# Optimization experiments

Hardware: AMD Instinct MI355X
Metric: run time of the kernel (lower is better)

Reference implementation:

```python
import jax, jax.numpy as jnp
import numpy as np

DIM = 64
NUM_GRAPHS = 256  # B: number of graphs in the batch (static)


def setup_inputs() -> dict:
    key = jax.random.key(0)
    ks = jax.random.split(key, 16)
    N, E = 8000, 40000

    def p(k, shape, s=0.1):
        return jax.random.normal(k, shape, jnp.float32) * s

    return dict(
        x=jax.random.normal(ks[0], (N, 21), jnp.float32),
        edge_attr=jax.random.uniform(ks[1], (E, 16), jnp.float32),
        edge_index=jax.random.randint(ks[2], (2, E), 0, N, jnp.int32),
        batch=jnp.sort(jax.random.randint(ks[3], (N,), 0, NUM_GRAPHS, jnp.int32)),
        lin0_w=p(ks[4], (DIM, 21)), lin0_b=jnp.zeros((DIM,), jnp.float32),
        nn_w1=p(ks[5], (128, 16)), nn_b1=jnp.zeros((128,), jnp.float32),
        nn_w2=p(ks[6], (DIM * DIM, 128), 0.02), nn_b2=jnp.zeros((DIM * DIM,), jnp.float32),
        conv_root=p(ks[7], (DIM, DIM)), conv_bias=jnp.zeros((DIM,), jnp.float32),
        gru_w_ih=p(ks[8], (3 * DIM, DIM)), gru_w_hh=p(ks[9], (3 * DIM, DIM)),
        gru_b_ih=jnp.zeros((3 * DIM,), jnp.float32), gru_b_hh=jnp.zeros((3 * DIM,), jnp.float32),
        lstm_w_ih=p(ks[10], (4 * DIM, 2 * DIM)), lstm_w_hh=p(ks[11], (4 * DIM, DIM)),
        lstm_b_ih=jnp.zeros((4 * DIM,), jnp.float32), lstm_b_hh=jnp.zeros((4 * DIM,), jnp.float32),
        lin1_w=p(ks[12], (DIM, 2 * DIM)), lin1_b=jnp.zeros((DIM,), jnp.float32),
        lin2_w=p(ks[13], (1, DIM)), lin2_b=jnp.zeros((1,), jnp.float32),
    )


def reference(x, edge_attr, edge_index, batch,
              lin0_w, lin0_b, nn_w1, nn_b1, nn_w2, nn_b2,
              conv_root, conv_bias, gru_w_ih, gru_w_hh, gru_b_ih, gru_b_hh,
              lstm_w_ih, lstm_w_hh, lstm_b_ih, lstm_b_hh,
              lin1_w, lin1_b, lin2_w, lin2_b):
    N = x.shape[0]
    src, dst = edge_index[0], edge_index[1]

    out = jax.nn.relu(x @ lin0_w.T + lin0_b)           # [N, 64]
    h = out

    # edge-conditioned weights (same every iteration): [E, 64, 64]
    e_h = jax.nn.relu(edge_attr @ nn_w1.T + nn_b1)
    w_e = (e_h @ nn_w2.T + nn_b2).reshape(-1, DIM, DIM)

    deg = jax.ops.segment_sum(jnp.ones_like(src, jnp.float32), dst, num_segments=N)
    deg = jnp.maximum(deg, 1.0)[:, None]

    for _ in range(3):
        # NNConv: gather + per-edge matmul + scatter-mean + root/bias
        msg = jnp.einsum('ei,eio->eo', out[src], w_e)  # [E, 64]
        agg = jax.ops.segment_sum(msg, dst, num_segments=N) / deg
        m = jax.nn.relu(agg + out @ conv_root + conv_bias)
        # GRU cell (seq_len = 1), torch gate order r, z, n
        gi = m @ gru_w_ih.T + gru_b_ih
        gh = h @ gru_w_hh.T + gru_b_hh
        ir, iz, i_n = jnp.split(gi, 3, axis=-1)
        hr, hz, h_n = jnp.split(gh, 3, axis=-1)
        r = jax.nn.sigmoid(ir + hr)
        z = jax.nn.sigmoid(iz + hz)
        n = jnp.tanh(i_n + r * h_n)
        h = (1.0 - z) * n + z * h
        out = h

    # Set2Set pooling, 3 processing steps
    B = NUM_GRAPHS
    q_star = jnp.zeros((B, 2 * DIM), x.dtype)
    hs = jnp.zeros((B, DIM), x.dtype)
    cs = jnp.zeros((B, DIM), x.dtype)
    for _ in range(3):
        gates = q_star @ lstm_w_ih.T + lstm_b_ih + hs @ lstm_w_hh.T + lstm_b_hh
        gi_, gf_, gg_, go_ = jnp.split(gates, 4, axis=-1)  # torch gate order i,f,g,o
        cs = jax.nn.sigmoid(gf_) * cs + jax.nn.sigmoid(gi_) * jnp.tanh(gg_)
        hs = jax.nn.sigmoid(go_) * jnp.tanh(cs)
        q = hs                                             # [B, 64]
        e = jnp.sum(out * q[batch], axis=-1)               # [N]
        mmax = jax.ops.segment_max(e, batch, num_segments=B)
        ex = jnp.exp(e - mmax[batch])
        s = jax.ops.segment_sum(ex, batch, num_segments=B)
        a = ex / s[batch]
        r_read = jax.ops.segment_sum(a[:, None] * out, batch, num_segments=B)
        q_star = jnp.concatenate([q, r_read], axis=-1)     # [B, 128]

    y = jax.nn.relu(q_star @ lin1_w.T + lin1_b)
    y = y @ lin2_w.T + lin2_b
    return y.reshape(-1)
```

## Files before the change

kernel.cpp:

```cpp
#include <hip/hip_runtime.h>
#include <math.h>

#define NN 8000
#define NE 40000
#define NGB 256
#define SK 8192
#define KSPLIT 16

typedef unsigned int u32;
typedef unsigned short u16;
typedef __attribute__((ext_vector_type(8))) short short8v;
typedef __attribute__((ext_vector_type(4))) float float4v;
typedef __attribute__((ext_vector_type(4))) unsigned int uint4v;

__device__ __forceinline__ float sigmoidf_(float x) { return 1.f / (1.f + expf(-x)); }

__device__ __forceinline__ u32 bf16_rne(float f) {
    u32 x = __builtin_bit_cast(u32, f);
    return (x + 0x7FFFu + ((x >> 16) & 1u)) >> 16;
}

__device__ __forceinline__ uint4v pack_bf8(const float v[8]) {
    u32 h[8];
#pragma unroll
    for (int j = 0; j < 8; ++j) h[j] = bf16_rne(v[j]);
    return (uint4v){ h[0] | (h[1] << 16), h[2] | (h[3] << 16),
                     h[4] | (h[5] << 16), h[6] | (h[7] << 16) };
}

__device__ __forceinline__ void pack8(const float* p, float scale, short8v& ah, short8v& al) {
    float v[8];
#pragma unroll
    for (int j = 0; j < 8; ++j) v[j] = p[j];
    u32 hu[8], lu[8];
#pragma unroll
    for (int j = 0; j < 8; ++j) {
        float s = v[j] * scale;
        hu[j] = bf16_rne(s);
        float fh = __builtin_bit_cast(float, hu[j] << 16);
        lu[j] = bf16_rne(s - fh);
    }
    uint4v hset = { hu[0] | (hu[1] << 16), hu[2] | (hu[3] << 16),
                    hu[4] | (hu[5] << 16), hu[6] | (hu[7] << 16) };
    uint4v lset = { lu[0] | (lu[1] << 16), lu[2] | (lu[3] << 16),
                    lu[4] | (lu[5] << 16), lu[6] | (lu[7] << 16) };
    ah = __builtin_bit_cast(short8v, hset);
    al = __builtin_bit_cast(short8v, lset);
}

#define SETUP_LIN0 (NN * 64)
#define SETUP_EH   (NE * 128)
#define SETUP_W2   (64 * SK)
#define SETUP_MW   8192
#define SETUP_GB   24576
__global__ void k_setup(const float* __restrict__ x, const float* __restrict__ lin0_w,
                        const float* __restrict__ lin0_b,
                        const float* __restrict__ ea, const float* __restrict__ nn_w1,
                        const float* __restrict__ nn_b1,
                        const float* __restrict__ nn_w2, const float* __restrict__ conv_root,
                        const float* __restrict__ nn_b2, const float* __restrict__ gw_ih,
                        const float* __restrict__ gw_hh, const int* __restrict__ batch,
                        float* __restrict__ out, float* __restrict__ e_h,
                        u16* __restrict__ Whi, u16* __restrict__ Wlo,
                        u16* __restrict__ Bmh, u16* __restrict__ Bml,
                        u16* __restrict__ Bih_h, u16* __restrict__ Bih_l,
                        u16* __restrict__ Bhh_h, u16* __restrict__ Bhh_l,
                        int* __restrict__ gstart) {
    int idx = blockIdx.x * 256 + threadIdx.x;
    if (idx < SETUP_LIN0) {
        int n = idx >> 6, o = idx & 63;
        float s = lin0_b[o];
#pragma unroll
        for (int c = 0; c < 21; ++c) s += x[n * 21 + c] * lin0_w[o * 21 + c];
        out[idx] = fmaxf(s, 0.f);
        return;
    }
    idx -= SETUP_LIN0;
    if (idx < SETUP_EH) {
        int e = idx >> 7, j = idx & 127;
        float s = nn_b1[j];
#pragma unroll
        for (int c = 0; c < 16; ++c) s += ea[e * 16 + c] * nn_w1[j * 16 + c];
        e_h[idx] = fmaxf(s, 0.f);
        return;
    }
    idx -= SETUP_EH;
    if (idx < SETUP_W2) {
        int o = idx >> 13, kap = idx & 8191;
        int i = kap >> 7, k = kap & 127;
        float v = nn_w2[(size_t)((i << 6) + o) * 128 + k];
        u32 h = bf16_rne(v);
        float fh = __builtin_bit_cast(float, h << 16);
        u32 l = bf16_rne(v - fh);
        int pos = ((kap >> 3) * 64 + o) * 8 + (kap & 7);
        Whi[pos] = (u16)h; Wlo[pos] = (u16)l;
        return;
    }
    idx -= SETUP_W2;
    if (idx < SETUP_MW) {
        int k = idx >> 6, o = idx & 63;
        float v = (k < 64) ? nn_b2[k * 64 + o] : conv_root[(k - 64) * 64 + o];
        u32 h = bf16_rne(v);
        float fh = __builtin_bit_cast(float, h << 16);
        u32 l = bf16_rne(v - fh);
        int pos = ((k >> 3) * 64 + o) * 8 + (k & 7);
        Bmh[pos] = (u16)h; Bml[pos] = (u16)l;
        return;
    }
    idx -= SETUP_MW;
    if (idx < SETUP_GB) {
        int half = idx >= 12288;
        int i2 = idx - half * 12288;
        int o = i2 % 192, k = i2 / 192;
        float v = half ? gw_hh[o * 64 + k] : gw_ih[o * 64 + k];
        u32 h = bf16_rne(v);
        float fh = __builtin_bit_cast(float, h << 16);
        u32 l = bf16_rne(v - fh);
        int pos = ((k >> 3) * 192 + o) * 8 + (k & 7);
        if (half) { Bhh_h[pos] = (u16)h; Bhh_l[pos] = (u16)l; }
        else      { Bih_h[pos] = (u16)h; Bih_l[pos] = (u16)l; }
        return;
    }
    idx -= SETUP_GB;
    if (idx <= NGB) {
        int g = idx;
        int lo = 0, hi = NN;
        while (lo < hi) { int mid = (lo + hi) >> 1; if (batch[mid] < g) lo = mid + 1; else hi = mid; }
        gstart[g] = lo;
    }
}
#define SETUP_TOTAL (SETUP_LIN0 + SETUP_EH + SETUP_W2 + SETUP_MW + SETUP_GB + NGB + 1)

__global__ void k_deg(const int* __restrict__ dst, int* __restrict__ degi) {
    int e = blockIdx.x * blockDim.x + threadIdx.x;
    if (e < NE) atomicAdd(&degi[dst[e]], 1);
}

__global__ __launch_bounds__(1024) void k_scan(
    const int* __restrict__ degi, int* __restrict__ rowptr,
    int* __restrict__ cursor, float* __restrict__ degf) {
    __shared__ int tsum[1024];
    int t = threadIdx.x;
    int base = t * 8;
    int v[8];
    int s = 0;
#pragma unroll
    for (int j = 0; j < 8; ++j) {
        int i = base + j;
        v[j] = (i < NN) ? degi[i] : 0;
        s += v[j];
    }
    tsum[t] = s;
    __syncthreads();
    for (int off = 1; off < 1024; off <<= 1) {
        int add = (t >= off) ? tsum[t - off] : 0;
        __syncthreads();
        tsum[t] += add;
        __syncthreads();
    }
    int exc = (t == 0) ? 0 : tsum[t - 1];
#pragma unroll
    for (int j = 0; j < 8; ++j) {
        int i = base + j;
        if (i < NN) {
            rowptr[i] = exc; cursor[i] = exc;
            degf[i] = (float)(v[j] > 1 ? v[j] : 1);
            exc += v[j];
        }
    }
    if (t == 1023) rowptr[NN] = tsum[1023];
}

__global__ void k_fill(const int* __restrict__ dst, int* __restrict__ cursor,
                       int* __restrict__ elist) {
    int e = blockIdx.x * blockDim.x + threadIdx.x;
    if (e < NE) { int p = atomicAdd(&cursor[dst[e]], 1); elist[p] = e; }
}

__global__ __launch_bounds__(256) void k_sbuild(
    const float* __restrict__ out, const float* __restrict__ e_h,
    const int* __restrict__ src, const int* __restrict__ rowptr,
    const int* __restrict__ elist, u16* __restrict__ S_bf,
    float* __restrict__ Osum, float* __restrict__ Psum, int base) {
    int t = threadIdx.x;
    int n = base + blockIdx.x;
    int ig = t >> 4;
    int k8 = t & 15;
    int lane = t & 63;
    float acc[4][8];
#pragma unroll
    for (int j = 0; j < 4; ++j)
#pragma unroll
        for (int c = 0; c < 8; ++c) acc[j][c] = 0.f;
    float osum = 0.f;
    int r0 = rowptr[n], r1 = rowptr[n + 1];
    const float4* out4 = (const float4*)out;
    const float4* eh4p = (const float4*)e_h;
    for (int idx = r0; idx < r1; ++idx) {
        int e = elist[idx];
        int sn = src[e];
        float4 e0 = eh4p[(size_t)e * 32 + k8 * 2];
        float4 e1 = eh4p[(size_t)e * 32 + k8 * 2 + 1];
        float ehv[8] = {e0.x, e0.y, e0.z, e0.w, e1.x, e1.y, e1.z, e1.w};
        float4 f = out4[sn * 16 + ig];
        float fv[4] = {f.x, f.y, f.z, f.w};
#pragma unroll
        for (int j = 0; j < 4; ++j)
#pragma unroll
            for (int c = 0; c < 8; ++c) acc[j][c] += fv[j] * ehv[c];
        if (t < 64) osum += out[(size_t)sn * 64 + lane];
    }
    uint4v* S4 = (uint4v*)S_bf;
    size_t rb = (size_t)blockIdx.x * (SK / 8);
#pragma unroll
    for (int j = 0; j < 4; ++j)
        S4[rb + (size_t)(ig * 4 + j) * 16 + k8] = pack_bf8(acc[j]);
    if (t < 64) {
        Osum[(size_t)n * 64 + lane] = osum;
        Psum[(size_t)n * 64 + lane] = 0.f;
    }
}

__global__ __launch_bounds__(128) void k_gemm(
    const u16* __restrict__ S_bf, const u16* __restrict__ Whi,
    const u16* __restrict__ Wlo, float* __restrict__ Psum, int base) {
    int t = threadIdx.x;
    int wv = t >> 6, lane = t & 63;
    int lrow = lane & 15, lkg = lane >> 4;
    int m0 = blockIdx.x * 64 + wv * 32;
    int ks = blockIdx.y;
    int kbase = ks * (SK / KSPLIT);
    float4v acc[2][4];
#pragma unroll
    for (int ms = 0; ms < 2; ++ms)
#pragma unroll
        for (int nt = 0; nt < 4; ++nt) acc[ms][nt] = (float4v){0.f, 0.f, 0.f, 0.f};
    const short8v* bhv = (const short8v*)Whi;
    const short8v* blv = (const short8v*)Wlo;
    const u16* ar0 = S_bf + (size_t)(m0 + lrow) * SK + kbase + lkg * 8;
    const u16* ar1 = ar0 + (size_t)16 * SK;
    int kc0 = (kbase >> 3) + lkg;

#pragma unroll 4
    for (int kk = 0; kk < SK / KSPLIT / 32; ++kk) {
        short8v ah0 = *(const short8v*)(ar0 + kk * 32);
        short8v ah1 = *(const short8v*)(ar1 + kk * 32);
        int bo = (kc0 + kk * 4) * 64 + lrow;
        short8v bh[4], bl[4];
#pragma unroll
        for (int nt = 0; nt < 4; ++nt) { bh[nt] = bhv[bo + nt * 16]; bl[nt] = blv[bo + nt * 16]; }
#pragma unroll
        for (int nt = 0; nt < 4; ++nt) {
            acc[0][nt] = __builtin_amdgcn_mfma_f32_16x16x32_bf16(ah0, bh[nt], acc[0][nt], 0, 0, 0);
            acc[0][nt] = __builtin_amdgcn_mfma_f32_16x16x32_bf16(ah0, bl[nt], acc[0][nt], 0, 0, 0);
            acc[1][nt] = __builtin_amdgcn_mfma_f32_16x16x32_bf16(ah1, bh[nt], acc[1][nt], 0, 0, 0);
            acc[1][nt] = __builtin_amdgcn_mfma_f32_16x16x32_bf16(ah1, bl[nt], acc[1][nt], 0, 0, 0);
        }
    }
    int gbase = base + m0;
#pragma unroll
    for (int ms = 0; ms < 2; ++ms)
#pragma unroll
        for (int nt = 0; nt < 4; ++nt)
#pragma unroll
            for (int jj = 0; jj < 4; ++jj) {
                int row = ms * 16 + lkg * 4 + jj;
                int o = nt * 16 + lrow;
                atomicAdd(&Psum[(size_t)(gbase + row) * 64 + o], acc[ms][nt][jj]);
            }
}

__global__ __launch_bounds__(64) void k_node(
    float* __restrict__ out, const float* __restrict__ Psum,
    const float* __restrict__ Osum, const float* __restrict__ degf,
    const u16* __restrict__ Bmh, const u16* __restrict__ Bml,
    const u16* __restrict__ Bih_h, const u16* __restrict__ Bih_l,
    const u16* __restrict__ Bhh_h, const u16* __restrict__ Bhh_l,
    const float* __restrict__ conv_bias,
    const float* __restrict__ gb_ih, const float* __restrict__ gb_hh) {
    __shared__ float lds[16][68];
    int lane = threadIdx.x;
    int lrow = lane & 15, lkg = lane >> 4;
    int n0 = blockIdx.x * 16;
    int arow = n0 + lrow;

    float invd = 1.f / degf[arow];
    float4v acc[4];
#pragma unroll
    for (int nt = 0; nt < 4; ++nt) acc[nt] = (float4v){0.f, 0.f, 0.f, 0.f};
    const short8v* bhv = (const short8v*)Bmh;
    const short8v* blv = (const short8v*)Bml;
#pragma unroll
    for (int s = 0; s < 4; ++s) {
        short8v ah, al;
        if (s < 2) pack8(&Osum[(size_t)arow * 64 + s * 32 + lkg * 8], invd, ah, al);
        else       pack8(&out[(size_t)arow * 64 + (s - 2) * 32 + lkg * 8], 1.f, ah, al);
        int kc = s * 4 + lkg;
#pragma unroll
        for (int nt = 0; nt < 4; ++nt) {
            short8v bh = bhv[kc * 64 + nt * 16 + lrow];
            short8v bl = blv[kc * 64 + nt * 16 + lrow];
            acc[nt] = __builtin_amdgcn_mfma_f32_16x16x32_bf16(ah, bh, acc[nt], 0, 0, 0);
            acc[nt] = __builtin_amdgcn_mfma_f32_16x16x32_bf16(al, bh, acc[nt], 0, 0, 0);
            acc[nt] = __builtin_amdgcn_mfma_f32_16x16x32_bf16(ah, bl, acc[nt], 0, 0, 0);
        }
    }
    float invd2[4];
#pragma unroll
    for (int jj = 0; jj < 4; ++jj) invd2[jj] = 1.f / degf[n0 + lkg * 4 + jj];
#pragma unroll
    for (int nt = 0; nt < 4; ++nt) {
        int o = nt * 16 + lrow;
        float cb = conv_bias[o];
#pragma unroll
        for (int jj = 0; jj < 4; ++jj) {
            int row = n0 + lkg * 4 + jj;
            lds[lkg * 4 + jj][o] =
                fmaxf(acc[nt][jj] + Psum[(size_t)row * 64 + o] * invd2[jj] + cb, 0.f);
        }
    }
    __syncthreads();

    float4v ai[12], ah_[12];
#pragma unroll
    for (int nt = 0; nt < 12; ++nt) { ai[nt] = (float4v){0.f, 0.f, 0.f, 0.f}; ah_[nt] = (float4v){0.f, 0.f, 0.f, 0.f}; }
    const short8v* bih_h = (const short8v*)Bih_h;
    const short8v* bih_l = (const short8v*)Bih_l;
    const short8v* bhh_h = (const short8v*)Bhh_h;
    const short8v* bhh_l = (const short8v*)Bhh_l;
#pragma unroll
    for (int s = 0; s < 2; ++s) {
        short8v mh, ml, hh, hl;
        pack8(&lds[lrow][s * 32 + lkg * 8], 1.f, mh, ml);
        pack8(&out[(size_t)arow * 64 + s * 32 + lkg * 8], 1.f, hh, hl);
        int kc = s * 4 + lkg;
#pragma unroll
        for (int nt = 0; nt < 12; ++nt) {
            int bo = kc * 192 + nt * 16 + lrow;
            short8v b1 = bih_h[bo], b2 = bih_l[bo];
            ai[nt] = __builtin_amdgcn_mfma_f32_16x16x32_bf16(mh, b1, ai[nt], 0, 0, 0);
            ai[nt] = __builtin_amdgcn_mfma_f32_16x16x32_bf16(ml, b1, ai[nt], 0, 0, 0);
            ai[nt] = __builtin_amdgcn_mfma_f32_16x16x32_bf16(mh, b2, ai[nt], 0, 0, 0);
            short8v b3 = bhh_h[bo], b4 = bhh_l[bo];
            ah_[nt] = __builtin_amdgcn_mfma_f32_16x16x32_bf16(hh, b3, ah_[nt], 0, 0, 0);
            ah_[nt] = __builtin_amdgcn_mfma_f32_16x16x32_bf16(hl, b3, ah_[nt], 0, 0, 0);
            ah_[nt] = __builtin_amdgcn_mfma_f32_16x16x32_bf16(hh, b4, ah_[nt], 0, 0, 0);
        }
    }
#pragma unroll
    for (int nt = 0; nt < 4; ++nt) {
        int o = nt * 16 + lrow;
        float bi0 = gb_ih[o], bi1 = gb_ih[64 + o], bi2 = gb_ih[128 + o];
        float bh0 = gb_hh[o], bh1 = gb_hh[64 + o], bh2 = gb_hh[128 + o];
#pragma unroll
        for (int jj = 0; jj < 4; ++jj) {
            int row = n0 + lkg * 4 + jj;
            float ir = ai[nt][jj] + bi0,  hr = ah_[nt][jj] + bh0;
            float iz = ai[nt + 4][jj] + bi1, hz = ah_[nt + 4][jj] + bh1;
            float in_ = ai[nt + 8][jj] + bi2, hn = ah_[nt + 8][jj] + bh2;
            float r = sigmoidf_(ir + hr);
            float z = sigmoidf_(iz + hz);
            float nv = tanhf(in_ + r * hn);
            float ho = out[(size_t)row * 64 + o];
            out[(size_t)row * 64 + o] = (1.f - z) * nv + z * ho;
        }
    }
}

__global__ __launch_bounds__(256) void k_s2s(
    const float* __restrict__ out, const int* __restrict__ gstart,
    const float* __restrict__ lw_ih, const float* __restrict__ lw_hh,
    const float* __restrict__ lb_ih, const float* __restrict__ lb_hh,
    const float* __restrict__ lin1_w, const float* __restrict__ lin1_b,
    const float* __restrict__ lin2_w, const float* __restrict__ lin2_b,
    float* __restrict__ yout) {
    __shared__ float qs[128], hsL[64], csL[64], gates[256];
    __shared__ float pv[384];
    __shared__ float red[4][64];
    __shared__ float sswv[4], mmaxw[4];
    int g = blockIdx.x, t = threadIdx.x, wv = t >> 6, lane = t & 63;
    int s0 = gstart[g], s1 = gstart[g + 1];
    if (t < 128) qs[t] = 0.f;
    if (t < 64) { hsL[t] = 0.f; csL[t] = 0.f; }
    __syncthreads();
    for (int st = 0; st < 3; ++st) {
        float s = lb_ih[t] + lb_hh[t];
        const float4* wi = (const float4*)&lw_ih[t * 128];
#pragma unroll
        for (int i = 0; i < 32; ++i) {
            float4 a = wi[i];
            s += qs[i * 4] * a.x + qs[i * 4 + 1] * a.y + qs[i * 4 + 2] * a.z + qs[i * 4 + 3] * a.w;
        }
        const float4* wh = (const float4*)&lw_hh[t * 64];
#pragma unroll
        for (int i = 0; i < 16; ++i) {
            float4 a = wh[i];
            s += hsL[i * 4] * a.x + hsL[i * 4 + 1] * a.y + hsL[i * 4 + 2] * a.z + hsL[i * 4 + 3] * a.w;
        }
        gates[t] = s;
        __syncthreads();
        if (t < 64) {
            float ig = sigmoidf_(gates[t]);
            float fg = sigmoidf_(gates[64 + t]);
            float gg = tanhf(gates[128 + t]);
            float og = sigmoidf_(gates[192 + t]);
            float c = fg * csL[t] + ig * gg;
            csL[t] = c;
            hsL[t] = og * tanhf(c);
        }
        __syncthreads();
        float wmax = -1e30f;
        for (int i = s0 + wv; i < s1; i += 4) {
            float p = out[(size_t)i * 64 + lane] * hsL[lane];
#pragma unroll
            for (int off = 32; off >= 1; off >>= 1) p += __shfl_xor(p, off);
            if (lane == 0) pv[i - s0] = p;
            wmax = fmaxf(wmax, p);
        }
        if (lane == 0) mmaxw[wv] = wmax;
        __syncthreads();
        float mmax = fmaxf(fmaxf(mmaxw[0], mmaxw[1]), fmaxf(mmaxw[2], mmaxw[3]));
        float ssum = 0.f, racc = 0.f;
        for (int i = s0 + wv; i < s1; i += 4) {
            float w = expf(pv[i - s0] - mmax);
            ssum += w;
            racc += w * out[(size_t)i * 64 + lane];
        }
        red[wv][lane] = racc;
        if (lane == 0) sswv[wv] = ssum;
        __syncthreads();
        if (t < 64) {
            float rt = red[0][t] + red[1][t] + red[2][t] + red[3][t];
            float stot = sswv[0] + sswv[1] + sswv[2] + sswv[3];
            qs[t] = hsL[t];
            qs[64 + t] = (s1 > s0) ? rt / stot : 0.f;
        }
        __syncthreads();
    }
    if (t < 64) {
        float s = lin1_b[t];
        const float4* w1 = (const float4*)&lin1_w[t * 128];
#pragma unroll
        for (int i = 0; i < 32; ++i) {
            float4 a = w1[i];
            s += qs[i * 4] * a.x + qs[i * 4 + 1] * a.y + qs[i * 4 + 2] * a.z + qs[i * 4 + 3] * a.w;
        }
        s = fmaxf(s, 0.f) * lin2_w[t];
#pragma unroll
        for (int off = 32; off >= 1; off >>= 1) s += __shfl_xor(s, off);
        if (t == 0) yout[g] = s + lin2_b[0];
    }
}

extern "C" void kernel_launch(void* const* d_in, const int* in_sizes, int n_in,
                              void* d_out, int out_size, void* d_ws, size_t ws_size,
                              hipStream_t stream) {
    (void)in_sizes; (void)n_in; (void)out_size;
    const float* x        = (const float*)d_in[0];
    const float* eattr    = (const float*)d_in[1];
    const int*   ei       = (const int*)d_in[2];
    const int*   batch    = (const int*)d_in[3];
    const float* lin0_w   = (const float*)d_in[4];
    const float* lin0_b   = (const float*)d_in[5];
    const float* nn_w1    = (const float*)d_in[6];
    const float* nn_b1    = (const float*)d_in[7];
    const float* nn_w2    = (const float*)d_in[8];
    const float* nn_b2    = (const float*)d_in[9];
    const float* conv_root= (const float*)d_in[10];
    const float* conv_bias= (const float*)d_in[11];
    const float* gw_ih    = (const float*)d_in[12];
    const float* gw_hh    = (const float*)d_in[13];
    const float* gb_ih    = (const float*)d_in[14];
    const float* gb_hh    = (const float*)d_in[15];
    const float* lw_ih    = (const float*)d_in[16];
    const float* lw_hh    = (const float*)d_in[17];
    const float* lb_ih    = (const float*)d_in[18];
    const float* lb_hh    = (const float*)d_in[19];
    const float* lin1_w   = (const float*)d_in[20];
    const float* lin1_b   = (const float*)d_in[21];
    const float* lin2_w   = (const float*)d_in[22];
    const float* lin2_b   = (const float*)d_in[23];
    const int* src = ei;
    const int* dst = ei + NE;

    char* w = (char*)d_ws;
    auto alloc = [&](size_t bytes) { char* p = w; w += (bytes + 255) & ~(size_t)255; return p; };
    float* out    = (float*)alloc((size_t)NN * 64 * 4);
    float* e_h    = (float*)alloc((size_t)NE * 128 * 4);
    u16*   Whi    = (u16*)alloc((size_t)64 * SK * 2);
    u16*   Wlo    = (u16*)alloc((size_t)64 * SK * 2);
    float* Psum   = (float*)alloc((size_t)NN * 64 * 4);
    float* Osum   = (float*)alloc((size_t)NN * 64 * 4);
    u16*   Bmh    = (u16*)alloc((size_t)8192 * 2);
    u16*   Bml    = (u16*)alloc((size_t)8192 * 2);
    u16*   Bih_h  = (u16*)alloc((size_t)12288 * 2);
    u16*   Bih_l  = (u16*)alloc((size_t)12288 * 2);
    u16*   Bhh_h  = (u16*)alloc((size_t)12288 * 2);
    u16*   Bhh_l  = (u16*)alloc((size_t)12288 * 2);
    float* degf   = (float*)alloc((size_t)NN * 4);
    int*   degi   = (int*)alloc((size_t)NN * 4);
    int*   rowptr = (int*)alloc((size_t)(NN + 1) * 4);
    int*   cursor = (int*)alloc((size_t)(NN + 1) * 4);
    int*   elist  = (int*)alloc((size_t)NE * 4);
    int*   gstart = (int*)alloc((size_t)(NGB + 1) * 4);
    size_t used = (size_t)(w - (char*)d_ws);
    size_t avail = ws_size > used ? ws_size - used : 0;
    size_t maxrows = avail / ((size_t)SK * 2);
    int chunkN = maxrows > (size_t)NN ? NN : (int)maxrows;
    chunkN = (chunkN / 64) * 64;
    if (chunkN < 64) chunkN = 64;
    u16* S_bf = (u16*)w;

    hipMemsetAsync(degi, 0, (size_t)NN * 4, stream);

    k_setup<<<(SETUP_TOTAL + 255) / 256, 256, 0, stream>>>(
        x, lin0_w, lin0_b, eattr, nn_w1, nn_b1, nn_w2, conv_root, nn_b2,
        gw_ih, gw_hh, batch, out, e_h, Whi, Wlo, Bmh, Bml,
        Bih_h, Bih_l, Bhh_h, Bhh_l, gstart);
    k_deg<<<(NE + 255) / 256, 256, 0, stream>>>(dst, degi);
    k_scan<<<1, 1024, 0, stream>>>(degi, rowptr, cursor, degf);
    k_fill<<<(NE + 255) / 256, 256, 0, stream>>>(dst, cursor, elist);

    for (int it = 0; it < 3; ++it) {
        for (int cb = 0; cb < NN; cb += chunkN) {
            int cn = (NN - cb) < chunkN ? (NN - cb) : chunkN;
            k_sbuild<<<cn, 256, 0, stream>>>(out, e_h, src, rowptr, elist, S_bf, Osum, Psum, cb);
            k_gemm<<<dim3(cn / 64, KSPLIT), 128, 0, stream>>>(S_bf, Whi, Wlo, Psum, cb);
        }
        k_node<<<NN / 16, 64, 0, stream>>>(out, Psum, Osum, degf, Bmh, Bml,
                                           Bih_h, Bih_l, Bhh_h, Bhh_l,
                                           conv_bias, gb_ih, gb_hh);
    }

    k_s2s<<<NGB, 256, 0, stream>>>(out, gstart, lw_ih, lw_hh, lb_ih, lb_hh,
                                   lin1_w, lin1_b, lin2_w, lin2_b, (float*)d_out);
}
```

Before: 411.6 us.

## Replace split-K atomic accumulation with per-split partial buffers reduced in node kernel

The GEMM no longer atomically adds its split-K partial results into a shared Psum. Each split now writes to its own slice of a KSPLIT-sized partial buffer, and the node kernel sums the 16 partials into LDS before using them. The GEMM block also shrinks from two waves to one (32 rows per block), which doubles the grid, and the degree memset is folded into the setup kernel. This trades atomic contention and the Psum zeroing for more memory traffic: 16 full-size partial buffers are written and then read back in k_node.

```diff
diff --git a/kernel.cpp b/kernel.cpp
--- a/kernel.cpp
+++ b/kernel.cpp
@@ -53,6 +53,8 @@
 #define SETUP_W2   (64 * SK)
 #define SETUP_MW   8192
 #define SETUP_GB   24576
+#define SETUP_G    (NGB + 1)
+#define SETUP_TOTAL (SETUP_LIN0 + SETUP_EH + SETUP_W2 + SETUP_MW + SETUP_GB + SETUP_G + NN)
 __global__ void k_setup(const float* __restrict__ x, const float* __restrict__ lin0_w,
                         const float* __restrict__ lin0_b,
                         const float* __restrict__ ea, const float* __restrict__ nn_w1,
@@ -65,7 +67,7 @@
                         u16* __restrict__ Bmh, u16* __restrict__ Bml,
                         u16* __restrict__ Bih_h, u16* __restrict__ Bih_l,
                         u16* __restrict__ Bhh_h, u16* __restrict__ Bhh_l,
-                        int* __restrict__ gstart) {
+                        int* __restrict__ gstart, int* __restrict__ degi) {
     int idx = blockIdx.x * 256 + threadIdx.x;
     if (idx < SETUP_LIN0) {
         int n = idx >> 6, o = idx & 63;
@@ -122,14 +124,16 @@
         return;
     }
     idx -= SETUP_GB;
-    if (idx <= NGB) {
+    if (idx < SETUP_G) {
         int g = idx;
         int lo = 0, hi = NN;
         while (lo < hi) { int mid = (lo + hi) >> 1; if (batch[mid] < g) lo = mid + 1; else hi = mid; }
         gstart[g] = lo;
-    }
-}
-#define SETUP_TOTAL (SETUP_LIN0 + SETUP_EH + SETUP_W2 + SETUP_MW + SETUP_GB + NGB + 1)
+        return;
+    }
+    idx -= SETUP_G;
+    if (idx < NN) degi[idx] = 0;
+}
 
 __global__ void k_deg(const int* __restrict__ dst, int* __restrict__ degi) {
     int e = blockIdx.x * blockDim.x + threadIdx.x;
@@ -181,7 +185,7 @@
     const float* __restrict__ out, const float* __restrict__ e_h,
     const int* __restrict__ src, const int* __restrict__ rowptr,
     const int* __restrict__ elist, u16* __restrict__ S_bf,
-    float* __restrict__ Osum, float* __restrict__ Psum, int base) {
+    float* __restrict__ Osum, int base) {
     int t = threadIdx.x;
     int n = base + blockIdx.x;
     int ig = t >> 4;
@@ -215,19 +219,15 @@
 #pragma unroll
     for (int j = 0; j < 4; ++j)
         S4[rb + (size_t)(ig * 4 + j) * 16 + k8] = pack_bf8(acc[j]);
-    if (t < 64) {
-        Osum[(size_t)n * 64 + lane] = osum;
-        Psum[(size_t)n * 64 + lane] = 0.f;
-    }
-}
-
-__global__ __launch_bounds__(128) void k_gemm(
+    if (t < 64) Osum[(size_t)n * 64 + lane] = osum;
+}
+
+__global__ __launch_bounds__(64) void k_gemm(
     const u16* __restrict__ S_bf, const u16* __restrict__ Whi,
-    const u16* __restrict__ Wlo, float* __restrict__ Psum, int base) {
-    int t = threadIdx.x;
-    int wv = t >> 6, lane = t & 63;
+    const u16* __restrict__ Wlo, float* __restrict__ P, int base) {
+    int lane = threadIdx.x;
     int lrow = lane & 15, lkg = lane >> 4;
-    int m0 = blockIdx.x * 64 + wv * 32;
+    int m0 = blockIdx.x * 32;
     int ks = blockIdx.y;
     int kbase = ks * (SK / KSPLIT);
     float4v acc[2][4];
@@ -266,12 +266,12 @@
             for (int jj = 0; jj < 4; ++jj) {
                 int row = ms * 16 + lkg * 4 + jj;
                 int o = nt * 16 + lrow;
-                atomicAdd(&Psum[(size_t)(gbase + row) * 64 + o], acc[ms][nt][jj]);
+                P[((size_t)ks * NN + gbase + row) * 64 + o] = acc[ms][nt][jj];
             }
 }
 
 __global__ __launch_bounds__(64) void k_node(
-    float* __restrict__ out, const float* __restrict__ Psum,
+    float* __restrict__ out, const float* __restrict__ P,
     const float* __restrict__ Osum, const float* __restrict__ degf,
     const u16* __restrict__ Bmh, const u16* __restrict__ Bml,
     const u16* __restrict__ Bih_h, const u16* __restrict__ Bih_l,
@@ -284,6 +284,24 @@
     int n0 = blockIdx.x * 16;
     int arow = n0 + lrow;
 
+    {
+        const float4* P4 = (const float4*)P;
+        float4 ps[4];
+#pragma unroll
+        for (int c = 0; c < 4; ++c) ps[c] = make_float4(0.f, 0.f, 0.f, 0.f);
+        for (int p = 0; p < KSPLIT; ++p) {
+#pragma unroll
+            for (int c = 0; c < 4; ++c) {
+                float4 v = P4[(size_t)p * (NN * 16) + (size_t)arow * 16 + lkg * 4 + c];
+                ps[c].x += v.x; ps[c].y += v.y; ps[c].z += v.z; ps[c].w += v.w;
+            }
+        }
+#pragma unroll
+        for (int c = 0; c < 4; ++c)
+            *(float4*)&lds[lrow][lkg * 16 + c * 4] = ps[c];
+    }
+    __syncthreads();
+
     float invd = 1.f / degf[arow];
     float4v acc[4];
 #pragma unroll
@@ -308,17 +326,21 @@
     float invd2[4];
 #pragma unroll
     for (int jj = 0; jj < 4; ++jj) invd2[jj] = 1.f / degf[n0 + lkg * 4 + jj];
+    float mval[4][4];
 #pragma unroll
     for (int nt = 0; nt < 4; ++nt) {
         int o = nt * 16 + lrow;
         float cb = conv_bias[o];
 #pragma unroll
-        for (int jj = 0; jj < 4; ++jj) {
-            int row = n0 + lkg * 4 + jj;
-            lds[lkg * 4 + jj][o] =
-                fmaxf(acc[nt][jj] + Psum[(size_t)row * 64 + o] * invd2[jj] + cb, 0.f);
-        }
-    }
+        for (int jj = 0; jj < 4; ++jj)
+            mval[nt][jj] = fmaxf(acc[nt][jj] + lds[lkg * 4 + jj][o] * invd2[jj] + cb, 0.f);
+    }
+    __syncthreads();
+#pragma unroll
+    for (int nt = 0; nt < 4; ++nt)
+#pragma unroll
+        for (int jj = 0; jj < 4; ++jj)
+            lds[lkg * 4 + jj][nt * 16 + lrow] = mval[nt][jj];
     __syncthreads();
 
     float4v ai[12], ah_[12];
@@ -489,7 +511,7 @@
     float* e_h    = (float*)alloc((size_t)NE * 128 * 4);
     u16*   Whi    = (u16*)alloc((size_t)64 * SK * 2);
     u16*   Wlo    = (u16*)alloc((size_t)64 * SK * 2);
-    float* Psum   = (float*)alloc((size_t)NN * 64 * 4);
+    float* P      = (float*)alloc((size_t)KSPLIT * NN * 64 * 4);
     float* Osum   = (float*)alloc((size_t)NN * 64 * 4);
     u16*   Bmh    = (u16*)alloc((size_t)8192 * 2);
     u16*   Bml    = (u16*)alloc((size_t)8192 * 2);
@@ -511,12 +533,10 @@
     if (chunkN < 64) chunkN = 64;
     u16* S_bf = (u16*)w;
 
-    hipMemsetAsync(degi, 0, (size_t)NN * 4, stream);
-
     k_setup<<<(SETUP_TOTAL + 255) / 256, 256, 0, stream>>>(
         x, lin0_w, lin0_b, eattr, nn_w1, nn_b1, nn_w2, conv_root, nn_b2,
         gw_ih, gw_hh, batch, out, e_h, Whi, Wlo, Bmh, Bml,
-        Bih_h, Bih_l, Bhh_h, Bhh_l, gstart);
+        Bih_h, Bih_l, Bhh_h, Bhh_l, gstart, degi);
     k_deg<<<(NE + 255) / 256, 256, 0, stream>>>(dst, degi);
     k_scan<<<1, 1024, 0, stream>>>(degi, rowptr, cursor, degf);
     k_fill<<<(NE + 255) / 256, 256, 0, stream>>>(dst, cursor, elist);
@@ -524,10 +544,10 @@
     for (int it = 0; it < 3; ++it) {
         for (int cb = 0; cb < NN; cb += chunkN) {
             int cn = (NN - cb) < chunkN ? (NN - cb) : chunkN;
-            k_sbuild<<<cn, 256, 0, stream>>>(out, e_h, src, rowptr, elist, S_bf, Osum, Psum, cb);
-            k_gemm<<<dim3(cn / 64, KSPLIT), 128, 0, stream>>>(S_bf, Whi, Wlo, Psum, cb);
-        }
-        k_node<<<NN / 16, 64, 0, stream>>>(out, Psum, Osum, degf, Bmh, Bml,
+            k_sbuild<<<cn, 256, 0, stream>>>(out, e_h, src, rowptr, elist, S_bf, Osum, cb);
+            k_gemm<<<dim3(cn / 32, KSPLIT), 64, 0, stream>>>(S_bf, Whi, Wlo, P, cb);
+        }
+        k_node<<<NN / 16, 64, 0, stream>>>(out, P, Osum, degf, Bmh, Bml,
                                            Bih_h, Bih_l, Bhh_h, Bhh_l,
                                            conv_bias, gb_ih, gb_hh);
     }
```

New measurement: 380.1 us. -7.7%, faster.

## Fuse per-node S construction with bf16 MFMA GEMM through shared memory

Applied to the files above, without the earlier changes.

Replaces the two-kernel scheme, which wrote a large bf16 S matrix to global memory and then ran a K-split GEMM with atomic adds, with one kernel. Each block of 16 nodes builds its S slice in shared memory one K chunk at a time and feeds it straight into MFMA. This removes the global S round trip, the Psum zeroing and the atomics, and the W reordering in setup is adjusted to the new K ordering. The trade-offs are that each block walks its edge lists 16 times (once per K chunk), uses 16-row tiles, and synchronises twice per chunk. The degree memset is also folded into the setup kernel.

```diff
diff --git a/kernel.cpp b/kernel.cpp
--- a/kernel.cpp
+++ b/kernel.cpp
@@ -5,7 +5,6 @@
 #define NE 40000
 #define NGB 256
 #define SK 8192
-#define KSPLIT 16
 
 typedef unsigned int u32;
 typedef unsigned short u16;
@@ -18,14 +17,6 @@
 __device__ __forceinline__ u32 bf16_rne(float f) {
     u32 x = __builtin_bit_cast(u32, f);
     return (x + 0x7FFFu + ((x >> 16) & 1u)) >> 16;
-}
-
-__device__ __forceinline__ uint4v pack_bf8(const float v[8]) {
-    u32 h[8];
-#pragma unroll
-    for (int j = 0; j < 8; ++j) h[j] = bf16_rne(v[j]);
-    return (uint4v){ h[0] | (h[1] << 16), h[2] | (h[3] << 16),
-                     h[4] | (h[5] << 16), h[6] | (h[7] << 16) };
 }
 
 __device__ __forceinline__ void pack8(const float* p, float scale, short8v& ah, short8v& al) {
@@ -53,6 +44,8 @@
 #define SETUP_W2   (64 * SK)
 #define SETUP_MW   8192
 #define SETUP_GB   24576
+#define SETUP_G    (NGB + 1)
+#define SETUP_TOTAL (SETUP_LIN0 + SETUP_EH + SETUP_W2 + SETUP_MW + SETUP_GB + SETUP_G + NN)
 __global__ void k_setup(const float* __restrict__ x, const float* __restrict__ lin0_w,
                         const float* __restrict__ lin0_b,
                         const float* __restrict__ ea, const float* __restrict__ nn_w1,
@@ -65,7 +58,7 @@
                         u16* __restrict__ Bmh, u16* __restrict__ Bml,
                         u16* __restrict__ Bih_h, u16* __restrict__ Bih_l,
                         u16* __restrict__ Bhh_h, u16* __restrict__ Bhh_l,
-                        int* __restrict__ gstart) {
+                        int* __restrict__ gstart, int* __restrict__ degi) {
     int idx = blockIdx.x * 256 + threadIdx.x;
     if (idx < SETUP_LIN0) {
         int n = idx >> 6, o = idx & 63;
@@ -87,7 +80,7 @@
     idx -= SETUP_EH;
     if (idx < SETUP_W2) {
         int o = idx >> 13, kap = idx & 8191;
-        int i = kap >> 7, k = kap & 127;
+        int k = kap >> 6, i = kap & 63;
         float v = nn_w2[(size_t)((i << 6) + o) * 128 + k];
         u32 h = bf16_rne(v);
         float fh = __builtin_bit_cast(float, h << 16);
@@ -122,14 +115,16 @@
         return;
     }
     idx -= SETUP_GB;
-    if (idx <= NGB) {
+    if (idx < SETUP_G) {
         int g = idx;
         int lo = 0, hi = NN;
         while (lo < hi) { int mid = (lo + hi) >> 1; if (batch[mid] < g) lo = mid + 1; else hi = mid; }
         gstart[g] = lo;
-    }
-}
-#define SETUP_TOTAL (SETUP_LIN0 + SETUP_EH + SETUP_W2 + SETUP_MW + SETUP_GB + NGB + 1)
+        return;
+    }
+    idx -= SETUP_G;
+    if (idx < NN) degi[idx] = 0;
+}
 
 __global__ void k_deg(const int* __restrict__ dst, int* __restrict__ degi) {
     int e = blockIdx.x * blockDim.x + threadIdx.x;
@@ -177,97 +172,68 @@
     if (e < NE) { int p = atomicAdd(&cursor[dst[e]], 1); elist[p] = e; }
 }
 
-__global__ __launch_bounds__(256) void k_sbuild(
+__global__ __launch_bounds__(256) void k_conv(
     const float* __restrict__ out, const float* __restrict__ e_h,
     const int* __restrict__ src, const int* __restrict__ rowptr,
-    const int* __restrict__ elist, u16* __restrict__ S_bf,
-    float* __restrict__ Osum, float* __restrict__ Psum, int base) {
+    const int* __restrict__ elist,
+    const u16* __restrict__ Whi, const u16* __restrict__ Wlo,
+    float* __restrict__ Osum, float* __restrict__ Psum) {
+    __shared__ u16 S_chunk[16][520];
     int t = threadIdx.x;
-    int n = base + blockIdx.x;
-    int ig = t >> 4;
-    int k8 = t & 15;
-    int lane = t & 63;
-    float acc[4][8];
-#pragma unroll
-    for (int j = 0; j < 4; ++j)
-#pragma unroll
-        for (int c = 0; c < 8; ++c) acc[j][c] = 0.f;
-    float osum = 0.f;
-    int r0 = rowptr[n], r1 = rowptr[n + 1];
+    int n0 = blockIdx.x * 16;
+    int r = t >> 4, c = t & 15;
+    int n = n0 + r;
+    int ei0 = rowptr[n], ei1 = rowptr[n + 1];
+    int lane = t & 63, w = t >> 6;
+    int lrow = lane & 15, lkg = lane >> 4;
+    float4v acc = (float4v){0.f, 0.f, 0.f, 0.f};
+    const short8v* bhv = (const short8v*)Whi;
+    const short8v* blv = (const short8v*)Wlo;
     const float4* out4 = (const float4*)out;
     const float4* eh4p = (const float4*)e_h;
-    for (int idx = r0; idx < r1; ++idx) {
-        int e = elist[idx];
-        int sn = src[e];
-        float4 e0 = eh4p[(size_t)e * 32 + k8 * 2];
-        float4 e1 = eh4p[(size_t)e * 32 + k8 * 2 + 1];
-        float ehv[8] = {e0.x, e0.y, e0.z, e0.w, e1.x, e1.y, e1.z, e1.w};
-        float4 f = out4[sn * 16 + ig];
-        float fv[4] = {f.x, f.y, f.z, f.w};
-#pragma unroll
-        for (int j = 0; j < 4; ++j)
-#pragma unroll
-            for (int c = 0; c < 8; ++c) acc[j][c] += fv[j] * ehv[c];
-        if (t < 64) osum += out[(size_t)sn * 64 + lane];
-    }
-    uint4v* S4 = (uint4v*)S_bf;
-    size_t rb = (size_t)blockIdx.x * (SK / 8);
-#pragma unroll
-    for (int j = 0; j < 4; ++j)
-        S4[rb + (size_t)(ig * 4 + j) * 16 + k8] = pack_bf8(acc[j]);
-    if (t < 64) {
-        Osum[(size_t)n * 64 + lane] = osum;
-        Psum[(size_t)n * 64 + lane] = 0.f;
-    }
-}
-
-__global__ __launch_bounds__(128) void k_gemm(
-    const u16* __restrict__ S_bf, const u16* __restrict__ Whi,
-    const u16* __restrict__ Wlo, float* __restrict__ Psum, int base) {
-    int t = threadIdx.x;
-    int wv = t >> 6, lane = t & 63;
-    int lrow = lane & 15, lkg = lane >> 4;
-    int m0 = blockIdx.x * 64 + wv * 32;
-    int ks = blockIdx.y;
-    int kbase = ks * (SK / KSPLIT);
-    float4v acc[2][4];
-#pragma unroll
-    for (int ms = 0; ms < 2; ++ms)
-#pragma unroll
-        for (int nt = 0; nt < 4; ++nt) acc[ms][nt] = (float4v){0.f, 0.f, 0.f, 0.f};
-    const short8v* bhv = (const short8v*)Whi;
-    const short8v* blv = (const short8v*)Wlo;
-    const u16* ar0 = S_bf + (size_t)(m0 + lrow) * SK + kbase + lkg * 8;
-    const u16* ar1 = ar0 + (size_t)16 * SK;
-    int kc0 = (kbase >> 3) + lkg;
-
+
+    for (int ks = 0; ks < 16; ++ks) {
+        float a[8][4];
+#pragma unroll
+        for (int kk = 0; kk < 8; ++kk)
+#pragma unroll
+            for (int j = 0; j < 4; ++j) a[kk][j] = 0.f;
+        float os[4] = {0.f, 0.f, 0.f, 0.f};
+        for (int idx = ei0; idx < ei1; ++idx) {
+            int e = elist[idx];
+            int sn = src[e];
+            float4 ea0 = eh4p[(size_t)e * 32 + ks * 2];
+            float4 ea1 = eh4p[(size_t)e * 32 + ks * 2 + 1];
+            float ehv[8] = {ea0.x, ea0.y, ea0.z, ea0.w, ea1.x, ea1.y, ea1.z, ea1.w};
+            float4 f = out4[(size_t)sn * 16 + c];
+            float fv[4] = {f.x, f.y, f.z, f.w};
+#pragma unroll
+            for (int kk = 0; kk < 8; ++kk)
+#pragma unroll
+                for (int j = 0; j < 4; ++j) a[kk][j] += ehv[kk] * fv[j];
+            if (ks == 0) { os[0] += fv[0]; os[1] += fv[1]; os[2] += fv[2]; os[3] += fv[3]; }
+        }
+#pragma unroll
+        for (int kk = 0; kk < 8; ++kk) {
+            u32 lo = bf16_rne(a[kk][0]) | (bf16_rne(a[kk][1]) << 16);
+            u32 hi = bf16_rne(a[kk][2]) | (bf16_rne(a[kk][3]) << 16);
+            *(uint2*)&S_chunk[r][kk * 64 + c * 4] = make_uint2(lo, hi);
+        }
+        if (ks == 0)
+            *(float4*)&Osum[(size_t)n * 64 + c * 4] = make_float4(os[0], os[1], os[2], os[3]);
+        __syncthreads();
 #pragma unroll 4
-    for (int kk = 0; kk < SK / KSPLIT / 32; ++kk) {
-        short8v ah0 = *(const short8v*)(ar0 + kk * 32);
-        short8v ah1 = *(const short8v*)(ar1 + kk * 32);
-        int bo = (kc0 + kk * 4) * 64 + lrow;
-        short8v bh[4], bl[4];
-#pragma unroll
-        for (int nt = 0; nt < 4; ++nt) { bh[nt] = bhv[bo + nt * 16]; bl[nt] = blv[bo + nt * 16]; }
-#pragma unroll
-        for (int nt = 0; nt < 4; ++nt) {
-            acc[0][nt] = __builtin_amdgcn_mfma_f32_16x16x32_bf16(ah0, bh[nt], acc[0][nt], 0, 0, 0);
-            acc[0][nt] = __builtin_amdgcn_mfma_f32_16x16x32_bf16(ah0, bl[nt], acc[0][nt], 0, 0, 0);
-            acc[1][nt] = __builtin_amdgcn_mfma_f32_16x16x32_bf16(ah1, bh[nt], acc[1][nt], 0, 0, 0);
-            acc[1][nt] = __builtin_amdgcn_mfma_f32_16x16x32_bf16(ah1, bl[nt], acc[1][nt], 0, 0, 0);
-        }
-    }
-    int gbase = base + m0;
-#pragma unroll
-    for (int ms = 0; ms < 2; ++ms)
-#pragma unroll
-        for (int nt = 0; nt < 4; ++nt)
-#pragma unroll
-            for (int jj = 0; jj < 4; ++jj) {
-                int row = ms * 16 + lkg * 4 + jj;
-                int o = nt * 16 + lrow;
-                atomicAdd(&Psum[(size_t)(gbase + row) * 64 + o], acc[ms][nt][jj]);
-            }
+        for (int kk2 = 0; kk2 < 16; ++kk2) {
+            short8v av = *(const short8v*)&S_chunk[lrow][kk2 * 32 + lkg * 8];
+            int bo = (ks * 64 + kk2 * 4 + lkg) * 64 + w * 16 + lrow;
+            acc = __builtin_amdgcn_mfma_f32_16x16x32_bf16(av, bhv[bo], acc, 0, 0, 0);
+            acc = __builtin_amdgcn_mfma_f32_16x16x32_bf16(av, blv[bo], acc, 0, 0, 0);
+        }
+        __syncthreads();
+    }
+#pragma unroll
+    for (int jj = 0; jj < 4; ++jj)
+        Psum[(size_t)(n0 + lkg * 4 + jj) * 64 + w * 16 + lrow] = acc[jj];
 }
 
 __global__ __launch_bounds__(64) void k_node(
@@ -455,7 +421,7 @@
 extern "C" void kernel_launch(void* const* d_in, const int* in_sizes, int n_in,
                               void* d_out, int out_size, void* d_ws, size_t ws_size,
                               hipStream_t stream) {
-    (void)in_sizes; (void)n_in; (void)out_size;
+    (void)in_sizes; (void)n_in; (void)out_size; (void)ws_size;
     const float* x        = (const float*)d_in[0];
     const float* eattr    = (const float*)d_in[1];
     const int*   ei       = (const int*)d_in[2];
@@ -503,30 +469,17 @@
     int*   cursor = (int*)alloc((size_t)(NN + 1) * 4);
     int*   elist  = (int*)alloc((size_t)NE * 4);
     int*   gstart = (int*)alloc((size_t)(NGB + 1) * 4);
-    size_t used = (size_t)(w - (char*)d_ws);
-    size_t avail = ws_size > used ? ws_size - used : 0;
-    size_t maxrows = avail / ((size_t)SK * 2);
-    int chunkN = maxrows > (size_t)NN ? NN : (int)maxrows;
-    chunkN = (chunkN / 64) * 64;
-    if (chunkN < 64) chunkN = 64;
-    u16* S_bf = (u16*)w;
-
-    hipMemsetAsync(degi, 0, (size_t)NN * 4, stream);
 
     k_setup<<<(SETUP_TOTAL + 255) / 256, 256, 0, stream>>>(
         x, lin0_w, lin0_b, eattr, nn_w1, nn_b1, nn_w2, conv_root, nn_b2,
         gw_ih, gw_hh, batch, out, e_h, Whi, Wlo, Bmh, Bml,
-        Bih_h, Bih_l, Bhh_h, Bhh_l, gstart);
+        Bih_h, Bih_l, Bhh_h, Bhh_l, gstart, degi);
     k_deg<<<(NE + 255) / 256, 256, 0, stream>>>(dst, degi);
     k_scan<<<1, 1024, 0, stream>>>(degi, rowptr, cursor, degf);
     k_fill<<<(NE + 255) / 256, 256, 0, stream>>>(dst, cursor, elist);
 
     for (int it = 0; it < 3; ++it) {
-        for (int cb = 0; cb < NN; cb += chunkN) {
-            int cn = (NN - cb) < chunkN ? (NN - cb) : chunkN;
-            k_sbuild<<<cn, 256, 0, stream>>>(out, e_h, src, rowptr, elist, S_bf, Osum, Psum, cb);
-            k_gemm<<<dim3(cn / 64, KSPLIT), 128, 0, stream>>>(S_bf, Whi, Wlo, Psum, cb);
-        }
+        k_conv<<<NN / 16, 256, 0, stream>>>(out, e_h, src, rowptr, elist, Whi, Wlo, Osum, Psum);
         k_node<<<NN / 16, 64, 0, stream>>>(out, Psum, Osum, degf, Bmh, Bml,
                                            Bih_h, Bih_l, Bhh_h, Bhh_l,
                                            conv_bias, gb_ih, gb_hh);
```

Measured after the change: 810.2 us. +96.8%, slower.
